# Optimization experiments

Hardware: AMD Instinct MI355X
Metric: run time of the kernel (lower is better)

The kernel has to match this reference:

```python
import jax, jax.numpy as jnp
import numpy as np

R = 16  # number of attention heads


def setup_inputs() -> dict:
    key = jax.random.key(0)
    ks = jax.random.split(key, 6)
    B, T, D = 2, 2048, 1024
    s = 1.0 / np.sqrt(D)
    return {
        "q": jax.random.normal(ks[0], (B, T, D), jnp.float32),
        "k": jax.random.normal(ks[1], (B, T, D), jnp.float32),
        "q_map": jax.random.normal(ks[2], (D, D), jnp.float32) * s,
        "k_map": jax.random.normal(ks[3], (D, D), jnp.float32) * s,
        "v_map": jax.random.normal(ks[4], (D, D), jnp.float32) * s,
        "output_map": jax.random.normal(ks[5], (D, D), jnp.float32) * s,
    }


def _split_heads(x, r):
    # [B, T, D] -> [B, r, T, D//r]
    B, T, D = x.shape
    return x.reshape(B, T, r, D // r).transpose(0, 2, 1, 3)


def reference(q, k, q_map, k_map, v_map, output_map):
    # v = k (the layer reuses Keys as Values)
    B, Tq, D = q.shape
    dh = D // R
    qh = _split_heads(q @ q_map, R)  # [B, r, Tq, dh]
    kh = _split_heads(k @ k_map, R)  # [B, r, Tk, dh]
    vh = _split_heads(k @ v_map, R)  # [B, r, Tk, dh]
    scale = 1.0 / jnp.sqrt(jnp.asarray(dh, qh.dtype))
    scores = jnp.einsum('brqd,brkd->brqk', qh, kh) * scale
    weights = jax.nn.softmax(scores, axis=-1)  # dropout=0 / inference -> identity
    out = jnp.einsum('brqk,brkd->brqd', weights, vh)  # [B, r, Tq, dh]
    merged = out.transpose(0, 2, 1, 3).reshape(B, Tq, D)
    return merged @ output_map
```

## Files before the change

kernel.cpp:

```cpp
#include <hip/hip_runtime.h>
#include <hip/hip_bf16.h>


typedef unsigned short u16;
typedef __attribute__((ext_vector_type(8))) short short8;
typedef __attribute__((ext_vector_type(4))) float f32x4;

__device__ __forceinline__ u16 f2bf(float f) {
  __hip_bfloat16 h = __float2bfloat16(f);
  return reinterpret_cast<u16&>(h);
}

__device__ __forceinline__ void storeC(float* C, size_t i, float v) { C[i] = v; }
__device__ __forceinline__ void storeC(u16* C, size_t i, float v) { C[i] = f2bf(v); }

__device__ __forceinline__ void gl_lds16(const u16* g, u16* l) {
  __builtin_amdgcn_global_load_lds(
      (const __attribute__((address_space(1))) void*)g,
      (__attribute__((address_space(3))) void*)l, 16, 0, 0);
}

template <int NW>
__device__ __forceinline__ void stage_tile(const u16* __restrict__ g, int gs,
                                           u16* lds, int rows, int wave, int lane) {
  const int lr8 = lane >> 3;
  const int gc = ((lane & 7) ^ lr8) * 8;
  const int issues = rows >> 3;
  for (int t = wave; t < issues; t += NW)
    gl_lds16(g + (size_t)(t * 8 + lr8) * gs + gc, lds + t * 512);
}

__global__ __launch_bounds__(256)
void convert_qk(const float4* __restrict__ q, const float4* __restrict__ k,
                u16* __restrict__ qb, u16* __restrict__ kb) {
  int i = blockIdx.x * 256 + threadIdx.x;
  float4 qv = q[i], kv = k[i];
  ushort4 qo, ko;
  qo.x = f2bf(qv.x); qo.y = f2bf(qv.y); qo.z = f2bf(qv.z); qo.w = f2bf(qv.w);
  ko.x = f2bf(kv.x); ko.y = f2bf(kv.y); ko.z = f2bf(kv.z); ko.w = f2bf(kv.w);
  reinterpret_cast<ushort4*>(qb)[i] = qo;
  reinterpret_cast<ushort4*>(kb)[i] = ko;
}

__global__ __launch_bounds__(256)
void convert_maps(const float* __restrict__ qm, const float* __restrict__ km,
                  const float* __restrict__ vm, const float* __restrict__ om,
                  u16* __restrict__ qmT, u16* __restrict__ kmT,
                  u16* __restrict__ vmT, u16* __restrict__ omT) {
  __shared__ float t[32][33];
  const float* src; u16* dst; float scale = 1.0f;
  switch (blockIdx.z) {
    case 0:  src = qm; dst = qmT; scale = 0.125f; break;
    case 1:  src = km; dst = kmT; break;
    case 2:  src = vm; dst = vmT; break;
    default: src = om; dst = omT; break;
  }
  int nb0 = blockIdx.x * 32, kb0 = blockIdx.y * 32;
  int c = threadIdx.x & 31, rq = threadIdx.x >> 5;
#pragma unroll
  for (int j = 0; j < 4; ++j) {
    int r = rq * 4 + j;
    t[r][c] = src[(size_t)(kb0 + r) * 1024 + nb0 + c];
  }
  __syncthreads();
#pragma unroll
  for (int j = 0; j < 4; ++j) {
    int nn = rq * 4 + j;
    dst[(size_t)(nb0 + nn) * 1024 + kb0 + c] = f2bf(t[c][nn] * scale);
  }
}

template <typename OutT>
__global__ __launch_bounds__(256)
void gemm_bt(const u16* __restrict__ A, const u16* __restrict__ Bt,
             OutT* __restrict__ C, int M, int N, int K) {
  __shared__ u16 As[2][128 * 64];
  __shared__ u16 Bs[2][64 * 64];
  const int tid = threadIdx.x;
  const int wave = tid >> 6, lane = tid & 63;
  const int lr = lane & 15, lg = lane >> 4;
  const int m0 = blockIdx.y * 128, n0 = blockIdx.x * 64;
  const int wm = (wave >> 1) * 64, wn = (wave & 1) * 32;

  f32x4 acc[4][2] = {};
  const int kT = K >> 6;
  const u16* Ab = A + (size_t)m0 * K;
  const u16* Bb = Bt + (size_t)n0 * K;

  stage_tile<4>(Ab, K, &As[0][0], 128, wave, lane);
  stage_tile<4>(Bb, K, &Bs[0][0], 64, wave, lane);
  __syncthreads();

  int cur = 0;
  for (int kt = 0; kt < kT; ++kt) {
    if (kt + 1 < kT) {
      stage_tile<4>(Ab + (kt + 1) * 64, K, &As[cur ^ 1][0], 128, wave, lane);
      stage_tile<4>(Bb + (kt + 1) * 64, K, &Bs[cur ^ 1][0], 64, wave, lane);
    }
#pragma unroll
    for (int ks = 0; ks < 2; ++ks) {
      short8 af[4], bfr[2];
#pragma unroll
      for (int i = 0; i < 4; ++i) {
        int ar = wm + i * 16 + lr;
        int ac = (ks * 4 + lg) ^ (ar & 7);
        af[i] = *reinterpret_cast<const short8*>(&As[cur][ar * 64 + ac * 8]);
      }
#pragma unroll
      for (int j = 0; j < 2; ++j) {
        int br = wn + j * 16 + lr;
        int bc = (ks * 4 + lg) ^ (br & 7);
        bfr[j] = *reinterpret_cast<const short8*>(&Bs[cur][br * 64 + bc * 8]);
      }
#pragma unroll
      for (int i = 0; i < 4; ++i)
#pragma unroll
        for (int j = 0; j < 2; ++j)
          acc[i][j] = __builtin_amdgcn_mfma_f32_16x16x32_bf16(af[i], bfr[j], acc[i][j], 0, 0, 0);
    }
    __syncthreads();
    cur ^= 1;
  }
#pragma unroll
  for (int i = 0; i < 4; ++i) {
    int row0 = m0 + wm + i * 16 + lg * 4;
#pragma unroll
    for (int j = 0; j < 2; ++j) {
      int col = n0 + wn + j * 16 + lr;
#pragma unroll
      for (int r = 0; r < 4; ++r)
        storeC(C, (size_t)(row0 + r) * N + col, acc[i][j][r]);
    }
  }
}

__global__ __launch_bounds__(256)
void transpose_v(const u16* __restrict__ KVp, u16* __restrict__ Vt) {
  __shared__ u16 t[64][72];
  const int kt = blockIdx.x, h = blockIdx.y, b = blockIdx.z;
  const int tid = threadIdx.x;
  const int r = tid >> 2, c = tid & 3;
  const u16* src = KVp + (size_t)(b * 2048 + kt * 64 + r) * 2048 + 1024 + h * 64;
  *reinterpret_cast<uint4*>(&t[r][c * 8]) = *reinterpret_cast<const uint4*>(src + c * 8);
  *reinterpret_cast<uint4*>(&t[r][(c + 4) * 8]) = *reinterpret_cast<const uint4*>(src + (c + 4) * 8);
  __syncthreads();
  u16* dst = Vt + (size_t)((b * 16 + h) * 64 + r) * 2048 + kt * 64;
  alignas(16) u16 tmp[8];
#pragma unroll
  for (int j = 0; j < 8; ++j) tmp[j] = t[c * 8 + j][r];
  *reinterpret_cast<uint4*>(dst + c * 8) = *reinterpret_cast<uint4*>(tmp);
#pragma unroll
  for (int j = 0; j < 8; ++j) tmp[j] = t[(c + 4) * 8 + j][r];
  *reinterpret_cast<uint4*>(dst + (c + 4) * 8) = *reinterpret_cast<uint4*>(tmp);
}

__global__ __launch_bounds__(256)
void attention(const u16* __restrict__ Qp, const u16* __restrict__ KVp,
               const u16* __restrict__ Vt, u16* __restrict__ merged) {
  __shared__ u16 Ks[2][64 * 64];
  __shared__ u16 Vs[2][64 * 64];
  __shared__ u16 Ps[128 * 64];
  const int tid = threadIdx.x;
  const int wave = tid >> 6, lane = tid & 63;
  const int lr = lane & 15, lg = lane >> 4;
  const int qt = blockIdx.x, h = blockIdx.y, b = blockIdx.z;
  const int q0 = qt * 128;

  short8 qf[2][2];
#pragma unroll
  for (int qm = 0; qm < 2; ++qm) {
    const size_t qrow = (size_t)(b * 2048 + q0 + wave * 32 + qm * 16 + lr);
#pragma unroll
    for (int ks = 0; ks < 2; ++ks)
      qf[qm][ks] = *reinterpret_cast<const short8*>(
          &Qp[qrow * 1024 + h * 64 + ks * 32 + lg * 8]);
  }

  f32x4 oacc[2][4] = {};
  float ell[2][4] = {};

  const u16* Kg = KVp + (size_t)(b * 2048) * 2048 + h * 64;
  const u16* Vg = Vt + (size_t)((b * 16 + h) * 64) * 2048;

  stage_tile<4>(Kg, 2048, &Ks[0][0], 64, wave, lane);
  stage_tile<4>(Vg, 2048, &Vs[0][0], 64, wave, lane);
  __syncthreads();

  int cur = 0;
  for (int ktile = 0; ktile < 32; ++ktile) {
    if (ktile + 1 < 32) {
      const int kn = (ktile + 1) * 64;
      stage_tile<4>(Kg + (size_t)kn * 2048, 2048, &Ks[cur ^ 1][0], 64, wave, lane);
      stage_tile<4>(Vg + kn, 2048, &Vs[cur ^ 1][0], 64, wave, lane);
    }
#pragma unroll
    for (int qm = 0; qm < 2; ++qm) {
#pragma unroll
      for (int kf = 0; kf < 4; ++kf) {
        f32x4 z = {};
#pragma unroll
        for (int ks = 0; ks < 2; ++ks) {
          int br = kf * 16 + lr;
          int bc = (ks * 4 + lg) ^ (br & 7);
          short8 kbf = *reinterpret_cast<const short8*>(&Ks[cur][br * 64 + bc * 8]);
          z = __builtin_amdgcn_mfma_f32_16x16x32_bf16(qf[qm][ks], kbf, z, 0, 0, 0);
        }
#pragma unroll
        for (int r = 0; r < 4; ++r) {
          float p = __expf(z[r]);
          ell[qm][r] += p;
          int qq = wave * 32 + qm * 16 + lg * 4 + r;
          int col = (kf * 16 + lr) ^ ((qq & 7) << 3);
          Ps[qq * 64 + col] = f2bf(p);
        }
      }
    }
    asm volatile("s_waitcnt lgkmcnt(0)" ::: "memory");
    __builtin_amdgcn_sched_barrier(0);
#pragma unroll
    for (int qm = 0; qm < 2; ++qm) {
#pragma unroll
      for (int ks = 0; ks < 2; ++ks) {
        int par = wave * 32 + qm * 16 + lr;
        int pac = (ks * 4 + lg) ^ (par & 7);
        short8 pa = *reinterpret_cast<const short8*>(&Ps[par * 64 + pac * 8]);
#pragma unroll
        for (int df = 0; df < 4; ++df) {
          int vr = df * 16 + lr;
          int vc = (ks * 4 + lg) ^ (vr & 7);
          short8 vb = *reinterpret_cast<const short8*>(&Vs[cur][vr * 64 + vc * 8]);
          oacc[qm][df] = __builtin_amdgcn_mfma_f32_16x16x32_bf16(pa, vb, oacc[qm][df], 0, 0, 0);
        }
      }
    }
    __syncthreads();
    cur ^= 1;
  }
#pragma unroll
  for (int qm = 0; qm < 2; ++qm) {
#pragma unroll
    for (int r = 0; r < 4; ++r) {
      float e = ell[qm][r];
      e += __shfl_xor(e, 1); e += __shfl_xor(e, 2);
      e += __shfl_xor(e, 4); e += __shfl_xor(e, 8);
      ell[qm][r] = 1.0f / e;
    }
    const size_t rowbase = (size_t)(b * 2048 + q0 + wave * 32 + qm * 16 + lg * 4);
#pragma unroll
    for (int df = 0; df < 4; ++df)
#pragma unroll
      for (int r = 0; r < 4; ++r)
        merged[(rowbase + r) * 1024 + h * 64 + df * 16 + lr] =
            f2bf(oacc[qm][df][r] * ell[qm][r]);
  }
}

extern "C" void kernel_launch(void* const* d_in, const int* in_sizes, int n_in,
                              void* d_out, int out_size, void* d_ws, size_t ws_size,
                              hipStream_t stream) {
  const float* q  = (const float*)d_in[0];
  const float* k  = (const float*)d_in[1];
  const float* qm = (const float*)d_in[2];
  const float* km = (const float*)d_in[3];
  const float* vm = (const float*)d_in[4];
  const float* om = (const float*)d_in[5];
  float* out = (float*)d_out;

  char* w = (char*)d_ws;
  const size_t MB = 1024 * 1024;
  u16* qb  = (u16*)(w + 0 * MB);
  u16* kb  = (u16*)(w + 8 * MB);
  u16* qmT = (u16*)(w + 16 * MB);
  u16* kmT = (u16*)(w + 18 * MB);
  u16* vmT = (u16*)(w + 20 * MB);
  u16* omT = (u16*)(w + 22 * MB);
  u16* Qp  = (u16*)(w + 24 * MB);
  u16* KVp = (u16*)(w + 32 * MB);
  u16* Vt  = (u16*)(w + 48 * MB);
  u16* merged = qb;

  convert_qk<<<4096, 256, 0, stream>>>((const float4*)q, (const float4*)k, qb, kb);
  convert_maps<<<dim3(32, 32, 4), 256, 0, stream>>>(qm, km, vm, om, qmT, kmT, vmT, omT);
  gemm_bt<u16><<<dim3(16, 32), 256, 0, stream>>>(qb, qmT, Qp, 4096, 1024, 1024);
  gemm_bt<u16><<<dim3(32, 32), 256, 0, stream>>>(kb, kmT, KVp, 4096, 2048, 1024);
  transpose_v<<<dim3(32, 16, 2), 256, 0, stream>>>(KVp, Vt);
  attention<<<dim3(16, 16, 2), 256, 0, stream>>>(Qp, KVp, Vt, merged);
  gemm_bt<float><<<dim3(16, 32), 256, 0, stream>>>(merged, omT, out, 4096, 1024, 1024);
}
```

Before: 238.2 us.

## Fuse V transpose into KV projection epilogue and transpose QK^T MFMA for packed P stores

New measurement: 219.1 us. -8.0%, faster.

```diff
diff --git a/kernel.cpp b/kernel.cpp
--- a/kernel.cpp
+++ b/kernel.cpp
@@ -10,9 +10,6 @@
   __hip_bfloat16 h = __float2bfloat16(f);
   return reinterpret_cast<u16&>(h);
 }
-
-__device__ __forceinline__ void storeC(float* C, size_t i, float v) { C[i] = v; }
-__device__ __forceinline__ void storeC(u16* C, size_t i, float v) { C[i] = f2bf(v); }
 
 __device__ __forceinline__ void gl_lds16(const u16* g, u16* l) {
   __builtin_amdgcn_global_load_lds(
@@ -20,14 +17,16 @@
       (__attribute__((address_space(3))) void*)l, 16, 0, 0);
 }
 
-template <int NW>
+template <int ROWS>
 __device__ __forceinline__ void stage_tile(const u16* __restrict__ g, int gs,
-                                           u16* lds, int rows, int wave, int lane) {
+                                           u16* lds, int wave, int lane) {
   const int lr8 = lane >> 3;
   const int gc = ((lane & 7) ^ lr8) * 8;
-  const int issues = rows >> 3;
-  for (int t = wave; t < issues; t += NW)
+#pragma unroll
+  for (int w = 0; w < ROWS / 32; ++w) {
+    int t = w * 4 + wave;
     gl_lds16(g + (size_t)(t * 8 + lr8) * gs + gc, lds + t * 512);
+  }
 }
 
 __global__ __launch_bounds__(256)
@@ -58,10 +57,8 @@
   int nb0 = blockIdx.x * 32, kb0 = blockIdx.y * 32;
   int c = threadIdx.x & 31, rq = threadIdx.x >> 5;
 #pragma unroll
-  for (int j = 0; j < 4; ++j) {
-    int r = rq * 4 + j;
-    t[r][c] = src[(size_t)(kb0 + r) * 1024 + nb0 + c];
-  }
+  for (int j = 0; j < 4; ++j)
+    t[rq * 4 + j][c] = src[(size_t)(kb0 + rq * 4 + j) * 1024 + nb0 + c];
   __syncthreads();
 #pragma unroll
   for (int j = 0; j < 4; ++j) {
@@ -70,36 +67,37 @@
   }
 }
 
-template <typename OutT>
-__global__ __launch_bounds__(256)
-void gemm_bt(const u16* __restrict__ A, const u16* __restrict__ Bt,
-             OutT* __restrict__ C, int M, int N, int K) {
+template <int BN, int MODE>
+__global__ __launch_bounds__(256)
+void gemm128(const u16* __restrict__ A, const u16* __restrict__ Bt,
+             void* __restrict__ Cv, u16* __restrict__ Vt, int K, int ldc) {
+  constexpr int JF = BN / 32;
   __shared__ u16 As[2][128 * 64];
-  __shared__ u16 Bs[2][64 * 64];
+  __shared__ u16 Bs[2][BN * 64];
   const int tid = threadIdx.x;
   const int wave = tid >> 6, lane = tid & 63;
   const int lr = lane & 15, lg = lane >> 4;
-  const int m0 = blockIdx.y * 128, n0 = blockIdx.x * 64;
-  const int wm = (wave >> 1) * 64, wn = (wave & 1) * 32;
-
-  f32x4 acc[4][2] = {};
+  const int m0 = blockIdx.y * 128, n0 = blockIdx.x * BN;
+  const int wm = (wave >> 1) * 64, wn = (wave & 1) * (BN / 2);
+
+  f32x4 acc[4][JF] = {};
   const int kT = K >> 6;
   const u16* Ab = A + (size_t)m0 * K;
   const u16* Bb = Bt + (size_t)n0 * K;
 
-  stage_tile<4>(Ab, K, &As[0][0], 128, wave, lane);
-  stage_tile<4>(Bb, K, &Bs[0][0], 64, wave, lane);
+  stage_tile<128>(Ab, K, &As[0][0], wave, lane);
+  stage_tile<BN>(Bb, K, &Bs[0][0], wave, lane);
   __syncthreads();
 
   int cur = 0;
   for (int kt = 0; kt < kT; ++kt) {
     if (kt + 1 < kT) {
-      stage_tile<4>(Ab + (kt + 1) * 64, K, &As[cur ^ 1][0], 128, wave, lane);
-      stage_tile<4>(Bb + (kt + 1) * 64, K, &Bs[cur ^ 1][0], 64, wave, lane);
+      stage_tile<128>(Ab + (kt + 1) * 64, K, &As[cur ^ 1][0], wave, lane);
+      stage_tile<BN>(Bb + (kt + 1) * 64, K, &Bs[cur ^ 1][0], wave, lane);
     }
 #pragma unroll
     for (int ks = 0; ks < 2; ++ks) {
-      short8 af[4], bfr[2];
+      short8 af[4], bfr[JF];
 #pragma unroll
       for (int i = 0; i < 4; ++i) {
         int ar = wm + i * 16 + lr;
@@ -107,7 +105,7 @@
         af[i] = *reinterpret_cast<const short8*>(&As[cur][ar * 64 + ac * 8]);
       }
 #pragma unroll
-      for (int j = 0; j < 2; ++j) {
+      for (int j = 0; j < JF; ++j) {
         int br = wn + j * 16 + lr;
         int bc = (ks * 4 + lg) ^ (br & 7);
         bfr[j] = *reinterpret_cast<const short8*>(&Bs[cur][br * 64 + bc * 8]);
@@ -115,47 +113,47 @@
 #pragma unroll
       for (int i = 0; i < 4; ++i)
 #pragma unroll
-        for (int j = 0; j < 2; ++j)
+        for (int j = 0; j < JF; ++j)
           acc[i][j] = __builtin_amdgcn_mfma_f32_16x16x32_bf16(af[i], bfr[j], acc[i][j], 0, 0, 0);
     }
     __syncthreads();
     cur ^= 1;
   }
+
 #pragma unroll
   for (int i = 0; i < 4; ++i) {
     int row0 = m0 + wm + i * 16 + lg * 4;
 #pragma unroll
-    for (int j = 0; j < 2; ++j) {
+    for (int j = 0; j < JF; ++j) {
       int col = n0 + wn + j * 16 + lr;
-#pragma unroll
-      for (int r = 0; r < 4; ++r)
-        storeC(C, (size_t)(row0 + r) * N + col, acc[i][j][r]);
-    }
-  }
-}
-
-__global__ __launch_bounds__(256)
-void transpose_v(const u16* __restrict__ KVp, u16* __restrict__ Vt) {
-  __shared__ u16 t[64][72];
-  const int kt = blockIdx.x, h = blockIdx.y, b = blockIdx.z;
-  const int tid = threadIdx.x;
-  const int r = tid >> 2, c = tid & 3;
-  const u16* src = KVp + (size_t)(b * 2048 + kt * 64 + r) * 2048 + 1024 + h * 64;
-  *reinterpret_cast<uint4*>(&t[r][c * 8]) = *reinterpret_cast<const uint4*>(src + c * 8);
-  *reinterpret_cast<uint4*>(&t[r][(c + 4) * 8]) = *reinterpret_cast<const uint4*>(src + (c + 4) * 8);
-  __syncthreads();
-  u16* dst = Vt + (size_t)((b * 16 + h) * 64 + r) * 2048 + kt * 64;
-  alignas(16) u16 tmp[8];
-#pragma unroll
-  for (int j = 0; j < 8; ++j) tmp[j] = t[c * 8 + j][r];
-  *reinterpret_cast<uint4*>(dst + c * 8) = *reinterpret_cast<uint4*>(tmp);
-#pragma unroll
-  for (int j = 0; j < 8; ++j) tmp[j] = t[(c + 4) * 8 + j][r];
-  *reinterpret_cast<uint4*>(dst + (c + 4) * 8) = *reinterpret_cast<uint4*>(tmp);
-}
-
-__global__ __launch_bounds__(256)
-void attention(const u16* __restrict__ Qp, const u16* __restrict__ KVp,
+      if (MODE == 2) {
+#pragma unroll
+        for (int r = 0; r < 4; ++r)
+          ((float*)Cv)[(size_t)(row0 + r) * ldc + col] = acc[i][j][r];
+      } else if (MODE == 0) {
+#pragma unroll
+        for (int r = 0; r < 4; ++r)
+          ((u16*)Cv)[(size_t)(row0 + r) * ldc + col] = f2bf(acc[i][j][r]);
+      } else {
+        if (n0 < 1024) {
+#pragma unroll
+          for (int r = 0; r < 4; ++r)
+            ((u16*)Cv)[(size_t)(row0 + r) * ldc + col] = f2bf(acc[i][j][r]);
+        } else {
+          int bb = row0 >> 11, kk = row0 & 2047;
+          int hd = col - 1024;
+          uint2 pk;
+          pk.x = (unsigned)f2bf(acc[i][j][0]) | ((unsigned)f2bf(acc[i][j][1]) << 16);
+          pk.y = (unsigned)f2bf(acc[i][j][2]) | ((unsigned)f2bf(acc[i][j][3]) << 16);
+          *reinterpret_cast<uint2*>(&Vt[(size_t)(bb * 1024 + hd) * 2048 + kk]) = pk;
+        }
+      }
+    }
+  }
+}
+
+__global__ __launch_bounds__(256)
+void attention(const u16* __restrict__ Qp, const u16* __restrict__ Kp,
                const u16* __restrict__ Vt, u16* __restrict__ merged) {
   __shared__ u16 Ks[2][64 * 64];
   __shared__ u16 Vs[2][64 * 64];
@@ -177,24 +175,25 @@
   }
 
   f32x4 oacc[2][4] = {};
-  float ell[2][4] = {};
-
-  const u16* Kg = KVp + (size_t)(b * 2048) * 2048 + h * 64;
-  const u16* Vg = Vt + (size_t)((b * 16 + h) * 64) * 2048;
-
-  stage_tile<4>(Kg, 2048, &Ks[0][0], 64, wave, lane);
-  stage_tile<4>(Vg, 2048, &Vs[0][0], 64, wave, lane);
+  float ell[2] = {0.f, 0.f};
+
+  const u16* Kg = Kp + (size_t)(b * 2048) * 1024 + h * 64;
+  const u16* Vg = Vt + (size_t)(b * 1024 + h * 64) * 2048;
+
+  stage_tile<64>(Kg, 1024, &Ks[0][0], wave, lane);
+  stage_tile<64>(Vg, 2048, &Vs[0][0], wave, lane);
   __syncthreads();
 
   int cur = 0;
   for (int ktile = 0; ktile < 32; ++ktile) {
     if (ktile + 1 < 32) {
       const int kn = (ktile + 1) * 64;
-      stage_tile<4>(Kg + (size_t)kn * 2048, 2048, &Ks[cur ^ 1][0], 64, wave, lane);
-      stage_tile<4>(Vg + kn, 2048, &Vs[cur ^ 1][0], 64, wave, lane);
+      stage_tile<64>(Kg + (size_t)kn * 1024, 1024, &Ks[cur ^ 1][0], wave, lane);
+      stage_tile<64>(Vg + kn, 2048, &Vs[cur ^ 1][0], wave, lane);
     }
 #pragma unroll
     for (int qm = 0; qm < 2; ++qm) {
+      const int qq = wave * 32 + qm * 16 + lr;
 #pragma unroll
       for (int kf = 0; kf < 4; ++kf) {
         f32x4 z = {};
@@ -203,16 +202,16 @@
           int br = kf * 16 + lr;
           int bc = (ks * 4 + lg) ^ (br & 7);
           short8 kbf = *reinterpret_cast<const short8*>(&Ks[cur][br * 64 + bc * 8]);
-          z = __builtin_amdgcn_mfma_f32_16x16x32_bf16(qf[qm][ks], kbf, z, 0, 0, 0);
+          z = __builtin_amdgcn_mfma_f32_16x16x32_bf16(kbf, qf[qm][ks], z, 0, 0, 0);
         }
-#pragma unroll
-        for (int r = 0; r < 4; ++r) {
-          float p = __expf(z[r]);
-          ell[qm][r] += p;
-          int qq = wave * 32 + qm * 16 + lg * 4 + r;
-          int col = (kf * 16 + lr) ^ ((qq & 7) << 3);
-          Ps[qq * 64 + col] = f2bf(p);
-        }
+        float p0 = __expf(z[0]), p1 = __expf(z[1]);
+        float p2 = __expf(z[2]), p3 = __expf(z[3]);
+        ell[qm] += (p0 + p1) + (p2 + p3);
+        uint2 pk;
+        pk.x = (unsigned)f2bf(p0) | ((unsigned)f2bf(p1) << 16);
+        pk.y = (unsigned)f2bf(p2) | ((unsigned)f2bf(p3) << 16);
+        int ch = (2 * kf + (lg >> 1)) ^ (qq & 7);
+        *reinterpret_cast<uint2*>(&Ps[qq * 64 + ch * 8 + (lg & 1) * 4]) = pk;
       }
     }
     asm volatile("s_waitcnt lgkmcnt(0)" ::: "memory");
@@ -238,20 +237,20 @@
   }
 #pragma unroll
   for (int qm = 0; qm < 2; ++qm) {
-#pragma unroll
-    for (int r = 0; r < 4; ++r) {
-      float e = ell[qm][r];
-      e += __shfl_xor(e, 1); e += __shfl_xor(e, 2);
-      e += __shfl_xor(e, 4); e += __shfl_xor(e, 8);
-      ell[qm][r] = 1.0f / e;
-    }
+    float e = ell[qm];
+    e += __shfl_xor(e, 16);
+    e += __shfl_xor(e, 32);
+    float inv = 1.0f / e;
+    float invr[4];
+#pragma unroll
+    for (int r = 0; r < 4; ++r) invr[r] = __shfl(inv, lg * 4 + r);
     const size_t rowbase = (size_t)(b * 2048 + q0 + wave * 32 + qm * 16 + lg * 4);
 #pragma unroll
     for (int df = 0; df < 4; ++df)
 #pragma unroll
       for (int r = 0; r < 4; ++r)
         merged[(rowbase + r) * 1024 + h * 64 + df * 16 + lr] =
-            f2bf(oacc[qm][df][r] * ell[qm][r]);
+            f2bf(oacc[qm][df][r] * invr[r]);
   }
 }
 
@@ -275,15 +274,14 @@
   u16* vmT = (u16*)(w + 20 * MB);
   u16* omT = (u16*)(w + 22 * MB);
   u16* Qp  = (u16*)(w + 24 * MB);
-  u16* KVp = (u16*)(w + 32 * MB);
+  u16* Kp  = (u16*)(w + 32 * MB);
   u16* Vt  = (u16*)(w + 48 * MB);
   u16* merged = qb;
 
   convert_qk<<<4096, 256, 0, stream>>>((const float4*)q, (const float4*)k, qb, kb);
   convert_maps<<<dim3(32, 32, 4), 256, 0, stream>>>(qm, km, vm, om, qmT, kmT, vmT, omT);
-  gemm_bt<u16><<<dim3(16, 32), 256, 0, stream>>>(qb, qmT, Qp, 4096, 1024, 1024);
-  gemm_bt<u16><<<dim3(32, 32), 256, 0, stream>>>(kb, kmT, KVp, 4096, 2048, 1024);
-  transpose_v<<<dim3(32, 16, 2), 256, 0, stream>>>(KVp, Vt);
-  attention<<<dim3(16, 16, 2), 256, 0, stream>>>(Qp, KVp, Vt, merged);
-  gemm_bt<float><<<dim3(16, 32), 256, 0, stream>>>(merged, omT, out, 4096, 1024, 1024);
-}
+  gemm128<64, 0><<<dim3(16, 32), 256, 0, stream>>>(qb, qmT, Qp, nullptr, 1024, 1024);
+  gemm128<128, 1><<<dim3(16, 32), 256, 0, stream>>>(kb, kmT, Kp, Vt, 1024, 1024);
+  attention<<<dim3(16, 16, 2), 256, 0, stream>>>(Qp, Kp, Vt, merged);
+  gemm128<64, 2><<<dim3(16, 32), 256, 0, stream>>>(merged, omT, out, nullptr, 1024, 1024);
+}
```
